# Performance work log

Measured on AMD Instinct MI355X. Metric: run time of the kernel, lower is better.

The kernel has to match this reference:

```python
import jax, jax.numpy as jnp
import numpy as np
import math

B, S, D = 4, 2048, 2048
NH, NKV, HD = 16, 4, 128

def setup_inputs() -> dict:
    key = jax.random.key(0)
    ks = jax.random.split(key, 9)
    s = 1.0 / math.sqrt(D)
    return {
        "x": jax.random.normal(ks[0], (B, S, D), dtype=jnp.float32),
        "Wq": jax.random.normal(ks[1], (D, NH * HD), dtype=jnp.float32) * s,
        "bq": jnp.zeros((NH * HD,), dtype=jnp.float32),
        "Wk": jax.random.normal(ks[2], (D, NKV * HD), dtype=jnp.float32) * s,
        "bk": jnp.zeros((NKV * HD,), dtype=jnp.float32),
        "Wv": jax.random.normal(ks[3], (D, NKV * HD), dtype=jnp.float32) * s,
        "bv": jnp.zeros((NKV * HD,), dtype=jnp.float32),
        "Wo": jax.random.normal(ks[4], (D, D), dtype=jnp.float32) * s,
        "bo": jnp.zeros((D,), dtype=jnp.float32),
    }

def reference(x, Wq, bq, Wk, bk, Wv, bv, Wo, bo):
    b, s, _ = x.shape
    group = NH // NKV
    q = (x @ Wq + bq).reshape(b, s, NH, HD).transpose(0, 2, 1, 3)   # [B,NH,S,HD]
    k = (x @ Wk + bk).reshape(b, s, NKV, HD).transpose(0, 2, 1, 3)  # [B,NKV,S,HD]
    v = (x @ Wv + bv).reshape(b, s, NKV, HD).transpose(0, 2, 1, 3)
    # repeat_interleave KV heads to match query heads
    k = jnp.repeat(k, group, axis=1)  # [B,NH,S,HD]
    v = jnp.repeat(v, group, axis=1)
    scores = jnp.einsum("bhqd,bhkd->bhqk", q, k) / math.sqrt(HD)
    causal = jnp.tril(jnp.ones((s, s), dtype=bool))
    scores = jnp.where(causal, scores, -jnp.inf)
    probs = jax.nn.softmax(scores, axis=-1)  # dropout p=0.0 -> identity
    out = jnp.einsum("bhqk,bhkd->bhqd", probs, v)
    out = out.transpose(0, 2, 1, 3).reshape(b, s, NH * HD)
    return out @ Wo + bo
```

## Files before the change

kernel.cpp:

```cpp
#include <hip/hip_runtime.h>
#include <hip/hip_bf16.h>

typedef __attribute__((ext_vector_type(4)))  float f32x4;
typedef __attribute__((ext_vector_type(16))) float f32x16;
typedef __attribute__((ext_vector_type(8)))  short s16x8;
typedef __attribute__((ext_vector_type(4)))  short s16x4;
typedef __attribute__((ext_vector_type(4)))  float fvec4;

__device__ __forceinline__ short f2bf(float f) {
    union { float f; unsigned u; } x; x.f = f;
    unsigned r = x.u + 0x7fffu + ((x.u >> 16) & 1u);
    return (short)(r >> 16);
}

__device__ __forceinline__ short cvtbf(float f) {
    __hip_bfloat16 t = __float2bfloat16(f);
    return *reinterpret_cast<short*>(&t);
}

__device__ __forceinline__ void gload_lds16(const short* g, short* lds) {
    __builtin_amdgcn_global_load_lds(
        (const __attribute__((address_space(1))) void*)g,
        (__attribute__((address_space(3))) void*)lds, 16, 0, 0);
}

__global__ __launch_bounds__(256) void prep(const float* __restrict__ x,
                                            const float* __restrict__ Wq,
                                            const float* __restrict__ Wk,
                                            const float* __restrict__ Wv,
                                            short* __restrict__ Xb,
                                            short* __restrict__ WqT,
                                            short* __restrict__ WkvT) {
    const int bid = blockIdx.x, tid = threadIdx.x;
    if (bid < 8192) {
        size_t i = ((size_t)bid * 256 + tid) * 8;
        fvec4 a = *(const fvec4*)&x[i];
        fvec4 b = *(const fvec4*)&x[i + 4];
        s16x8 o;
        o[0] = f2bf(a[0]); o[1] = f2bf(a[1]); o[2] = f2bf(a[2]); o[3] = f2bf(a[3]);
        o[4] = f2bf(b[0]); o[5] = f2bf(b[1]); o[6] = f2bf(b[2]); o[7] = f2bf(b[3]);
        *(s16x8*)&Xb[i] = o;
        return;
    }
    const float* W; short* Wt; int N, local;
    if (bid < 12288)      { W = Wq; Wt = WqT;                      N = 2048; local = bid - 8192; }
    else if (bid < 13312) { W = Wk; Wt = WkvT;                     N = 512;  local = bid - 12288; }
    else                  { W = Wv; Wt = WkvT + (size_t)512 * 2048; N = 512; local = bid - 13312; }
    __shared__ float tile[32][33];
    const int k0 = (local & 63) * 32, n0 = (local >> 6) * 32;
    const int tx = tid & 31, ty = tid >> 5;
    #pragma unroll
    for (int i = 0; i < 4; ++i) {
        int k = ty + i * 8;
        tile[k][tx] = W[(size_t)(k0 + k) * N + n0 + tx];
    }
    __syncthreads();
    #pragma unroll
    for (int i = 0; i < 4; ++i) {
        int n = ty + i * 8;
        Wt[(size_t)(n0 + n) * 2048 + k0 + tx] = f2bf(tile[tx][n]);
    }
}

__global__ __launch_bounds__(256) void tconv(const float* __restrict__ W,
                                             short* __restrict__ Wt,
                                             int K, int N) {
    __shared__ float tile[32][33];
    const int k0 = blockIdx.x * 32, n0 = blockIdx.y * 32;
    const int tx = threadIdx.x & 31, ty = threadIdx.x >> 5;
    #pragma unroll
    for (int i = 0; i < 4; ++i) {
        int k = ty + i * 8;
        tile[k][tx] = W[(size_t)(k0 + k) * N + n0 + tx];
    }
    __syncthreads();
    #pragma unroll
    for (int i = 0; i < 4; ++i) {
        int n = ty + i * 8;
        Wt[(size_t)(n0 + n) * K + k0 + tx] = f2bf(tile[tx][n]);
    }
}

template<int MODE>
__global__ __launch_bounds__(512, 1) void gemm256(const short* __restrict__ A,
                                                  const short* __restrict__ Bt,
                                                  const float* __restrict__ bias,
                                                  void* __restrict__ Cv,
                                                  int M, int N, int K) {
    __shared__ __align__(16) short As[2][16384];
    __shared__ __align__(16) short Bs[2][16384];
    const int tid = threadIdx.x, lane = tid & 63, w = tid >> 6;
    const int wr = w >> 2, wc = w & 3;
    const int lr = lane & 15, g = lane >> 4;
    const int bid = blockIdx.x;
    const int xcd = bid & 7, ii = bid >> 3;
    const int m0 = (xcd * 4 + (ii & 3)) * 256;
    const int n0 = (ii >> 2) * 256;
    const int r0 = w * 8 + (lane >> 3);
    const int sw = ((lane & 7) ^ ((lane >> 3) & 7)) * 8;
    const int swr = lr & 7;

    const short* ga = A  + (size_t)(m0 + r0) * K + sw;
    const short* gb = Bt + (size_t)(n0 + r0) * K + sw;

    f32x4 acc[8][4] = {};
    const int NT = K >> 6;

#define STAGE256(d, t) do {                                                     \
    const int kk0_ = (t) << 6;                                                  \
    _Pragma("unroll")                                                           \
    for (int it_ = 0; it_ < 4; ++it_) {                                         \
        gload_lds16(ga + (size_t)(it_ * 64) * K + kk0_, &As[d][it_ * 4096 + w * 512]); \
        gload_lds16(gb + (size_t)(it_ * 64) * K + kk0_, &Bs[d][it_ * 4096 + w * 512]); \
    }                                                                           \
} while (0)

    STAGE256(0, 0);

    for (int T = 0; T < NT; ++T) {
        const int d = T & 1;
        if (T + 1 < NT) {
            STAGE256((T + 1) & 1, T + 1);
            asm volatile("s_waitcnt vmcnt(8)" ::: "memory");
        } else {
            asm volatile("s_waitcnt vmcnt(0)" ::: "memory");
        }
        __builtin_amdgcn_s_barrier();
        __builtin_amdgcn_sched_barrier(0);
        s16x8 bf[4][2];
        #pragma unroll
        for (int n = 0; n < 4; ++n)
            #pragma unroll
            for (int kk = 0; kk < 2; ++kk)
                bf[n][kk] = *(const s16x8*)&Bs[d][(wc * 64 + n * 16 + lr) * 64 +
                                                 (((kk << 2) | g) ^ swr) * 8];
        #pragma unroll
        for (int p = 0; p < 4; ++p) {
            s16x8 af[2][2];
            #pragma unroll
            for (int mm = 0; mm < 2; ++mm)
                #pragma unroll
                for (int kk = 0; kk < 2; ++kk)
                    af[mm][kk] = *(const s16x8*)&As[d][(wr * 128 + (p * 2 + mm) * 16 + lr) * 64 +
                                                      (((kk << 2) | g) ^ swr) * 8];
            __builtin_amdgcn_s_barrier();
            asm volatile("s_waitcnt lgkmcnt(0)" ::: "memory");
            __builtin_amdgcn_sched_barrier(0);
            __builtin_amdgcn_s_setprio(1);
            #pragma unroll
            for (int kk = 0; kk < 2; ++kk)
                #pragma unroll
                for (int mm = 0; mm < 2; ++mm)
                    #pragma unroll
                    for (int n = 0; n < 4; ++n)
                        acc[p * 2 + mm][n] = __builtin_amdgcn_mfma_f32_16x16x32_bf16(
                            af[mm][kk], bf[n][kk], acc[p * 2 + mm][n], 0, 0, 0);
            __builtin_amdgcn_s_setprio(0);
            __builtin_amdgcn_s_barrier();
        }
        __builtin_amdgcn_sched_barrier(0);
    }
    #pragma unroll
    for (int m = 0; m < 8; ++m)
        #pragma unroll
        for (int j = 0; j < 4; ++j) {
            int row = m0 + wr * 128 + m * 16 + g * 4 + j;
            #pragma unroll
            for (int n = 0; n < 4; ++n) {
                int col = n0 + wc * 64 + n * 16 + lr;
                float v = acc[m][n][j] + bias[col];
                if constexpr (MODE == 1) ((short*)Cv)[(size_t)row * N + col] = f2bf(v);
                else                     ((float*)Cv)[(size_t)row * N + col] = v;
            }
        }
#undef STAGE256
}

__global__ __launch_bounds__(512, 1) void gemm256kv(const short* __restrict__ A,
                                                    const short* __restrict__ Bt,
                                                    const float* __restrict__ bias_k,
                                                    const float* __restrict__ bias_v,
                                                    short* __restrict__ Kout,
                                                    short* __restrict__ Vout,
                                                    int K) {
    __shared__ __align__(16) short As[2][16384];
    __shared__ __align__(16) short Bs[2][8192];
    const int tid = threadIdx.x, lane = tid & 63, w = tid >> 6;
    const int wr = w >> 1, wc = w & 1;
    const int lr = lane & 15, g = lane >> 4;
    const int bid = blockIdx.x;
    const int xcd = bid & 7, ii = bid >> 3;
    const int m0 = (xcd * 4 + (ii & 3)) * 256;
    const int n0 = (ii >> 2) * 128;
    const int r0 = w * 8 + (lane >> 3);
    const int sw = ((lane & 7) ^ ((lane >> 3) & 7)) * 8;
    const int swr = lr & 7;

    const short* ga = A  + (size_t)(m0 + r0) * K + sw;
    const short* gb = Bt + (size_t)(n0 + r0) * K + sw;

    f32x4 acc[4][4] = {};
    const int NT = K >> 6;

#define STAGEKV(d, t) do {                                                      \
    const int kk0_ = (t) << 6;                                                  \
    _Pragma("unroll")                                                           \
    for (int it_ = 0; it_ < 4; ++it_)                                           \
        gload_lds16(ga + (size_t)(it_ * 64) * K + kk0_, &As[d][it_ * 4096 + w * 512]); \
    _Pragma("unroll")                                                           \
    for (int it_ = 0; it_ < 2; ++it_)                                           \
        gload_lds16(gb + (size_t)(it_ * 64) * K + kk0_, &Bs[d][it_ * 4096 + w * 512]); \
} while (0)

    STAGEKV(0, 0);

    for (int T = 0; T < NT; ++T) {
        const int d = T & 1;
        if (T + 1 < NT) {
            STAGEKV((T + 1) & 1, T + 1);
            asm volatile("s_waitcnt vmcnt(6)" ::: "memory");
        } else {
            asm volatile("s_waitcnt vmcnt(0)" ::: "memory");
        }
        __builtin_amdgcn_s_barrier();
        __builtin_amdgcn_sched_barrier(0);
        s16x8 bf[4][2];
        #pragma unroll
        for (int n = 0; n < 4; ++n)
            #pragma unroll
            for (int kk = 0; kk < 2; ++kk)
                bf[n][kk] = *(const s16x8*)&Bs[d][(wc * 64 + n * 16 + lr) * 64 +
                                                 (((kk << 2) | g) ^ swr) * 8];
        #pragma unroll
        for (int p = 0; p < 2; ++p) {
            s16x8 af[2][2];
            #pragma unroll
            for (int mm = 0; mm < 2; ++mm)
                #pragma unroll
                for (int kk = 0; kk < 2; ++kk)
                    af[mm][kk] = *(const s16x8*)&As[d][(wr * 64 + (p * 2 + mm) * 16 + lr) * 64 +
                                                      (((kk << 2) | g) ^ swr) * 8];
            __builtin_amdgcn_s_barrier();
            asm volatile("s_waitcnt lgkmcnt(0)" ::: "memory");
            __builtin_amdgcn_sched_barrier(0);
            __builtin_amdgcn_s_setprio(1);
            #pragma unroll
            for (int kk = 0; kk < 2; ++kk)
                #pragma unroll
                for (int mm = 0; mm < 2; ++mm)
                    #pragma unroll
                    for (int n = 0; n < 4; ++n)
                        acc[p * 2 + mm][n] = __builtin_amdgcn_mfma_f32_16x16x32_bf16(
                            af[mm][kk], bf[n][kk], acc[p * 2 + mm][n], 0, 0, 0);
            __builtin_amdgcn_s_setprio(0);
            __builtin_amdgcn_s_barrier();
        }
        __builtin_amdgcn_sched_barrier(0);
    }
    if (n0 < 512) {
        #pragma unroll
        for (int m = 0; m < 4; ++m)
            #pragma unroll
            for (int j = 0; j < 4; ++j) {
                int row = m0 + wr * 64 + m * 16 + g * 4 + j;
                #pragma unroll
                for (int n = 0; n < 4; ++n) {
                    int col = n0 + wc * 64 + n * 16 + lr;
                    Kout[(size_t)row * 512 + col] = f2bf(acc[m][n][j] + bias_k[col]);
                }
            }
    } else {
        #pragma unroll
        for (int m = 0; m < 4; ++m)
            #pragma unroll
            for (int n = 0; n < 4; ++n) {
                int vcol = n0 - 512 + wc * 64 + n * 16 + lr;
                int kvh = vcol >> 7, dd = vcol & 127;
                int row0 = m0 + wr * 64 + m * 16 + g * 4;
                int b = row0 >> 11, s0 = row0 & 2047;
                int s0p = (s0 & ~15) | (((s0 >> 2) & 1) << 3) | (((s0 >> 3) & 1) << 2);
                s16x4 o;
                #pragma unroll
                for (int j = 0; j < 4; ++j) o[j] = f2bf(acc[m][n][j] + bias_v[vcol]);
                *(s16x4*)&Vout[(((size_t)b * 4 + kvh) * 128 + dd) * 2048 + s0p] = o;
            }
    }
#undef STAGEKV
}

#define SC2 0.12751743f

__global__ __launch_bounds__(512, 1) void attn_kernel(const short* __restrict__ Q,
                                                      const short* __restrict__ Kg,
                                                      const short* __restrict__ Vtg,
                                                      short* __restrict__ Oa) {
    __shared__ __align__(16) short Klds[2][8192];
    __shared__ __align__(16) short Vlds[2][8192];
    const int tid = threadIdx.x;
    const int lane = tid & 63, w = tid >> 6;
    const int l31 = lane & 31, hi = lane >> 5, e7 = lane & 7;
    const int ve = hi ^ e7;

    const int bid = blockIdx.x;
    const int grp = bid & 15, j = bid >> 4;
    const int b = grp >> 2, kvh = grp & 3;
    const int h = kvh * 4 + (j & 3);
    const int qtp = (j >> 2) & 3, ph = j >> 4;
    const int qt = ph ? (3 - qtp) : (4 + qtp);
    const int qb = qt << 8;

    const int q_min = qb + w * 32;
    const int qg = q_min + l31;
    const size_t qrow = (size_t)b * 2048 + qg;

    s16x8 qf[8];
    #pragma unroll
    for (int c = 0; c < 8; ++c)
        qf[c] = *(const s16x8*)&Q[qrow * 2048 + h * 128 + c * 16 + hi * 8];

    f32x16 oacc[4] = {};
    float m_run = -1e28f, l_half = 0.f;

    const int nt = (qb >> 6) + 4;

    const short* Kbase = Kg + ((size_t)b * 2048) * 512 + kvh * 128;
    const short* Vbase = Vtg + ((size_t)(b * 4 + kvh)) * 128 * 2048;

    const int krow0 = w * 4 + (lane >> 4), kslot = lane & 15;
    const int vrow0 = w * 8 + (lane >> 3), vslot = lane & 7;

#define STAGE(buf, t) do {                                                        \
    const int kv0_ = (t) << 6;                                                    \
    _Pragma("unroll")                                                             \
    for (int s_ = 0; s_ < 2; ++s_) {                                              \
        int kr = s_ * 32 + krow0;                                                 \
        gload_lds16(Kbase + (size_t)(kv0_ + kr) * 512 + (kslot ^ (kr & 7)) * 8,   \
                    &Klds[buf][s_ * 4096 + w * 512]);                             \
        int vr = s_ * 64 + vrow0;                                                 \
        gload_lds16(Vbase + (size_t)vr * 2048 + kv0_ + (vslot ^ (vr & 7)) * 8,    \
                    &Vlds[buf][s_ * 4096 + w * 512]);                             \
    }                                                                             \
} while (0)

#define SMPV(sv, st, domask) do {                                                 \
    if (domask) {                                                                 \
        _Pragma("unroll")                                                         \
        for (int r = 0; r < 16; ++r) {                                            \
            const int rw = (r & 3) + 8 * (r >> 2) + 4 * hi;                       \
            if (rw > l31) sv[r] = -1e30f;                                         \
        }                                                                         \
    }                                                                             \
    float mA = fmaxf(fmaxf(fmaxf(sv[0], sv[1]), fmaxf(sv[2], sv[3])),             \
                     fmaxf(fmaxf(sv[4], sv[5]), fmaxf(sv[6], sv[7])));            \
    float mB = fmaxf(fmaxf(fmaxf(sv[8], sv[9]), fmaxf(sv[10], sv[11])),           \
                     fmaxf(fmaxf(sv[12], sv[13]), fmaxf(sv[14], sv[15])));        \
    float pm = fmaxf(mA, mB);                                                     \
    pm = fmaxf(pm, __shfl_xor(pm, 32));                                           \
    if (!__all(pm <= m_run + 90.5f)) {                                            \
        float mn = fmaxf(m_run, pm);                                              \
        float fs = __builtin_amdgcn_exp2f((m_run - mn) * SC2);                    \
        l_half *= fs;                                                             \
        _Pragma("unroll")                                                         \
        for (int dn = 0; dn < 4; ++dn)                                            \
            _Pragma("unroll")                                                     \
            for (int r = 0; r < 16; ++r) oacc[dn][r] *= fs;                       \
        m_run = mn;                                                               \
    }                                                                             \
    const float mb2 = m_run * SC2;                                                \
    _Pragma("unroll")                                                             \
    for (int r = 0; r < 16; ++r)                                                  \
        sv[r] = __builtin_amdgcn_exp2f(fmaf(sv[r], SC2, -mb2));                   \
    l_half += (((sv[0] + sv[1]) + (sv[2] + sv[3])) +                              \
               ((sv[4] + sv[5]) + (sv[6] + sv[7]))) +                             \
              (((sv[8] + sv[9]) + (sv[10] + sv[11])) +                            \
               ((sv[12] + sv[13]) + (sv[14] + sv[15])));                          \
    s16x8 pa0, pa1;                                                               \
    _Pragma("unroll")                                                             \
    for (int jj = 0; jj < 8; ++jj) { pa0[jj] = cvtbf(sv[jj]); pa1[jj] = cvtbf(sv[8 + jj]); } \
    const short* vb = &Vlds[cur][l31 * 64];                                       \
    _Pragma("unroll")                                                             \
    for (int dn = 0; dn < 4; ++dn) {                                              \
        s16x8 vf = *(const s16x8*)&vb[dn * 2048 + ((((st) << 2) ^ ve)) * 8];      \
        oacc[dn] = __builtin_amdgcn_mfma_f32_32x32x16_bf16(vf, pa0, oacc[dn], 0, 0, 0); \
    }                                                                             \
    _Pragma("unroll")                                                             \
    for (int dn = 0; dn < 4; ++dn) {                                              \
        s16x8 vf = *(const s16x8*)&vb[dn * 2048 + (((((st) << 2) | 2) ^ ve)) * 8];\
        oacc[dn] = __builtin_amdgcn_mfma_f32_32x32x16_bf16(vf, pa1, oacc[dn], 0, 0, 0); \
    }                                                                             \
} while (0)

    STAGE(0, 0);
    __syncthreads();

    int cur = 0;
    for (int t = 0; t < nt; ++t) {
        if (t + 1 < nt) STAGE(cur ^ 1, t + 1);
        const int kv0 = t << 6;
        const bool w0 = kv0 <= q_min;
        const bool w1 = kv0 + 32 <= q_min;
        f32x16 s0 = {}, s1 = {};
        if (w0) {
            const short* kb = &Klds[cur][l31 * 128];
            #pragma unroll
            for (int c = 0; c < 8; ++c) {
                s16x8 kf = *(const s16x8*)&kb[(((c << 1) ^ ve)) * 8];
                s0 = __builtin_amdgcn_mfma_f32_32x32x16_bf16(kf, qf[c], s0, 0, 0, 0);
            }
        }
        if (w1) {
            const short* kb = &Klds[cur][(32 + l31) * 128];
            #pragma unroll
            for (int c = 0; c < 8; ++c) {
                s16x8 kf = *(const s16x8*)&kb[(((c << 1) ^ ve)) * 8];
                s1 = __builtin_amdgcn_mfma_f32_32x32x16_bf16(kf, qf[c], s1, 0, 0, 0);
            }
        }
        if (w0) SMPV(s0, 0, (kv0 == q_min));
        if (w1) SMPV(s1, 1, (kv0 + 32 == q_min));
        __syncthreads();
        cur ^= 1;
    }
    const float l_run = l_half + __shfl_xor(l_half, 32);
    const float inv = 1.0f / l_run;
    const size_t obase = qrow * 2048 + h * 128;
    #pragma unroll
    for (int dn = 0; dn < 4; ++dn)
        #pragma unroll
        for (int u = 0; u < 4; ++u) {
            s16x4 o;
            #pragma unroll
            for (int jj = 0; jj < 4; ++jj) o[jj] = cvtbf(oacc[dn][u * 4 + jj] * inv);
            *(s16x4*)&Oa[obase + dn * 32 + u * 8 + hi * 4] = o;
        }
#undef STAGE
#undef SMPV
}

extern "C" void kernel_launch(void* const* d_in, const int* in_sizes, int n_in,
                              void* d_out, int out_size, void* d_ws, size_t ws_size,
                              hipStream_t stream) {
    const float* x  = (const float*)d_in[0];
    const float* Wq = (const float*)d_in[1];
    const float* bq = (const float*)d_in[2];
    const float* Wk = (const float*)d_in[3];
    const float* bk = (const float*)d_in[4];
    const float* Wv = (const float*)d_in[5];
    const float* bv = (const float*)d_in[6];
    const float* Wo = (const float*)d_in[7];
    const float* bo = (const float*)d_in[8];
    float* out = (float*)d_out;

    char* ws = (char*)d_ws;
    short* Xb  = (short*)(ws);
    short* Qb  = (short*)(ws + (size_t)33554432);
    short* Kb  = (short*)(ws + (size_t)67108864);
    short* Vt  = (short*)(ws + (size_t)75497472);
    short* WoT = (short*)(ws);
    char* dob = (char*)d_out;
    short* WqT  = (short*)(dob);
    short* WkvT = (short*)(dob + (size_t)8388608);

    const int M = 8192, D = 2048;

    prep<<<dim3(14336), 256, 0, stream>>>(x, Wq, Wk, Wv, Xb, WqT, WkvT);

    gemm256<1><<<dim3(256), 512, 0, stream>>>(Xb, WqT, bq, Qb, M, 2048, D);
    gemm256kv<<<dim3(256), 512, 0, stream>>>(Xb, WkvT, bk, bv, Kb, Vt, D);

    tconv<<<dim3(64, 64), 256, 0, stream>>>(Wo, WoT, D, D);

    attn_kernel<<<dim3(512), 512, 0, stream>>>(Qb, Kb, Vt, Qb);

    gemm256<0><<<dim3(256), 512, 0, stream>>>(Qb, WoT, bo, out, M, 2048, D);
}
```

Before: 337.5 us.

## Interleave next-tile global loads across MFMA phases in the 256x256 GEMM

The 256x256 GEMM no longer issues all eight next-tile global-to-LDS loads at once. It now spreads them across the four MFMA sub-phases in pairs, with finer vmcnt waits, so the A chunks needed by the first two phases become ready before the later chunks finish. The aim is smoother memory traffic and earlier compute start. The KV GEMM also drops a workgroup barrier and an explicit lgkmcnt wait before its MFMA block, leaving the compiler to insert the waits. The cost is more barriers in the main GEMM and tighter hand-tuned wait counts that must match the exact issue order.

```diff
diff --git a/kernel.cpp b/kernel.cpp
--- a/kernel.cpp
+++ b/kernel.cpp
@@ -106,59 +106,76 @@
     f32x4 acc[8][4] = {};
     const int NT = K >> 6;
 
-#define STAGE256(d, t) do {                                                     \
-    const int kk0_ = (t) << 6;                                                  \
-    _Pragma("unroll")                                                           \
-    for (int it_ = 0; it_ < 4; ++it_) {                                         \
-        gload_lds16(ga + (size_t)(it_ * 64) * K + kk0_, &As[d][it_ * 4096 + w * 512]); \
-        gload_lds16(gb + (size_t)(it_ * 64) * K + kk0_, &Bs[d][it_ * 4096 + w * 512]); \
-    }                                                                           \
-} while (0)
-
-    STAGE256(0, 0);
+#define ISSUE_A(d, t, it) gload_lds16(ga + (size_t)((it) * 64) * K + ((t) << 6), \
+                                      &As[d][(it) * 4096 + w * 512])
+#define ISSUE_B(d, t, it) gload_lds16(gb + (size_t)((it) * 64) * K + ((t) << 6), \
+                                      &Bs[d][(it) * 4096 + w * 512])
+#define READ_AF(p)                                                               \
+    _Pragma("unroll")                                                            \
+    for (int mm = 0; mm < 2; ++mm)                                               \
+        _Pragma("unroll")                                                        \
+        for (int kk = 0; kk < 2; ++kk)                                           \
+            af[mm][kk] = *(const s16x8*)&As[d][(wr * 128 + ((p) * 2 + mm) * 16 + lr) * 64 + \
+                                              (((kk << 2) | g) ^ swr) * 8]
+#define MFMA_P(p)                                                                \
+    __builtin_amdgcn_s_setprio(1);                                               \
+    _Pragma("unroll")                                                            \
+    for (int kk = 0; kk < 2; ++kk)                                               \
+        _Pragma("unroll")                                                        \
+        for (int mm = 0; mm < 2; ++mm)                                           \
+            _Pragma("unroll")                                                    \
+            for (int n = 0; n < 4; ++n)                                          \
+                acc[(p) * 2 + mm][n] = __builtin_amdgcn_mfma_f32_16x16x32_bf16(  \
+                    af[mm][kk], bf[n][kk], acc[(p) * 2 + mm][n], 0, 0, 0);       \
+    __builtin_amdgcn_s_setprio(0)
+
+    ISSUE_B(0, 0, 0); ISSUE_B(0, 0, 1); ISSUE_B(0, 0, 2); ISSUE_B(0, 0, 3);
+    ISSUE_A(0, 0, 0); ISSUE_A(0, 0, 2); ISSUE_A(0, 0, 1); ISSUE_A(0, 0, 3);
 
     for (int T = 0; T < NT; ++T) {
-        const int d = T & 1;
-        if (T + 1 < NT) {
-            STAGE256((T + 1) & 1, T + 1);
-            asm volatile("s_waitcnt vmcnt(8)" ::: "memory");
-        } else {
-            asm volatile("s_waitcnt vmcnt(0)" ::: "memory");
-        }
-        __builtin_amdgcn_s_barrier();
-        __builtin_amdgcn_sched_barrier(0);
-        s16x8 bf[4][2];
+        const int d = T & 1, dn = d ^ 1;
+        const bool pf = (T + 1 < NT);
+        s16x8 bf[4][2], af[2][2];
+        if (pf) { ISSUE_B(dn, T + 1, 0); ISSUE_B(dn, T + 1, 1); }
+        if (pf) asm volatile("s_waitcnt vmcnt(4)" ::: "memory");
+        else    asm volatile("s_waitcnt vmcnt(2)" ::: "memory");
+        __builtin_amdgcn_s_barrier();
+        __builtin_amdgcn_sched_barrier(0);
         #pragma unroll
         for (int n = 0; n < 4; ++n)
             #pragma unroll
             for (int kk = 0; kk < 2; ++kk)
                 bf[n][kk] = *(const s16x8*)&Bs[d][(wc * 64 + n * 16 + lr) * 64 +
                                                  (((kk << 2) | g) ^ swr) * 8];
-        #pragma unroll
-        for (int p = 0; p < 4; ++p) {
-            s16x8 af[2][2];
-            #pragma unroll
-            for (int mm = 0; mm < 2; ++mm)
-                #pragma unroll
-                for (int kk = 0; kk < 2; ++kk)
-                    af[mm][kk] = *(const s16x8*)&As[d][(wr * 128 + (p * 2 + mm) * 16 + lr) * 64 +
-                                                      (((kk << 2) | g) ^ swr) * 8];
-            __builtin_amdgcn_s_barrier();
-            asm volatile("s_waitcnt lgkmcnt(0)" ::: "memory");
-            __builtin_amdgcn_sched_barrier(0);
-            __builtin_amdgcn_s_setprio(1);
-            #pragma unroll
-            for (int kk = 0; kk < 2; ++kk)
-                #pragma unroll
-                for (int mm = 0; mm < 2; ++mm)
-                    #pragma unroll
-                    for (int n = 0; n < 4; ++n)
-                        acc[p * 2 + mm][n] = __builtin_amdgcn_mfma_f32_16x16x32_bf16(
-                            af[mm][kk], bf[n][kk], acc[p * 2 + mm][n], 0, 0, 0);
-            __builtin_amdgcn_s_setprio(0);
-            __builtin_amdgcn_s_barrier();
-        }
-        __builtin_amdgcn_sched_barrier(0);
+        READ_AF(0);
+        asm volatile("s_waitcnt lgkmcnt(0)" ::: "memory");
+        __builtin_amdgcn_sched_barrier(0);
+        MFMA_P(0);
+        __builtin_amdgcn_s_barrier();
+        READ_AF(1);
+        if (pf) { ISSUE_B(dn, T + 1, 2); ISSUE_B(dn, T + 1, 3); }
+        __builtin_amdgcn_s_barrier();
+        asm volatile("s_waitcnt lgkmcnt(0)" ::: "memory");
+        __builtin_amdgcn_sched_barrier(0);
+        MFMA_P(1);
+        __builtin_amdgcn_s_barrier();
+        if (pf) { ISSUE_A(dn, T + 1, 0); ISSUE_A(dn, T + 1, 2); }
+        if (pf) asm volatile("s_waitcnt vmcnt(6)" ::: "memory");
+        else    asm volatile("s_waitcnt vmcnt(0)" ::: "memory");
+        __builtin_amdgcn_s_barrier();
+        __builtin_amdgcn_sched_barrier(0);
+        READ_AF(2);
+        asm volatile("s_waitcnt lgkmcnt(0)" ::: "memory");
+        __builtin_amdgcn_sched_barrier(0);
+        MFMA_P(2);
+        __builtin_amdgcn_s_barrier();
+        READ_AF(3);
+        if (pf) { ISSUE_A(dn, T + 1, 1); ISSUE_A(dn, T + 1, 3); }
+        __builtin_amdgcn_s_barrier();
+        asm volatile("s_waitcnt lgkmcnt(0)" ::: "memory");
+        __builtin_amdgcn_sched_barrier(0);
+        MFMA_P(3);
+        __builtin_amdgcn_s_barrier();
     }
     #pragma unroll
     for (int m = 0; m < 8; ++m)
@@ -173,7 +190,10 @@
                 else                     ((float*)Cv)[(size_t)row * N + col] = v;
             }
         }
-#undef STAGE256
+#undef ISSUE_A
+#undef ISSUE_B
+#undef READ_AF
+#undef MFMA_P
 }
 
 __global__ __launch_bounds__(512, 1) void gemm256kv(const short* __restrict__ A,
@@ -240,9 +260,6 @@
                 for (int kk = 0; kk < 2; ++kk)
                     af[mm][kk] = *(const s16x8*)&As[d][(wr * 64 + (p * 2 + mm) * 16 + lr) * 64 +
                                                       (((kk << 2) | g) ^ swr) * 8];
-            __builtin_amdgcn_s_barrier();
-            asm volatile("s_waitcnt lgkmcnt(0)" ::: "memory");
-            __builtin_amdgcn_sched_barrier(0);
             __builtin_amdgcn_s_setprio(1);
             #pragma unroll
             for (int kk = 0; kk < 2; ++kk)
```

Measured after the change: 335.4 us. Within noise of the previous version (-0.6%).
